# Kernel tuning notes

Measured on AMD Instinct MI355X. Metric: run time of the kernel, lower is better.

## Reference

```python
import jax, jax.numpy as jnp
import numpy as np

HEAD_DIM = 64
N_HEADS = 25
N_KV_HEADS = 5
WINDOW = 1024
N_META = 128
EPS = 1e-6
ROPE_BASE = 10000.0


def _rmsnorm(x, w):
    # per-head RMSNorm over last dim, computed in fp32 (matches HymbaRMSNorm)
    xf = x.astype(jnp.float32)
    var = jnp.mean(xf * xf, axis=-1, keepdims=True)
    return w * (xf * jax.lax.rsqrt(var + EPS)).astype(x.dtype)


def _rotate_half(x):
    x1, x2 = jnp.split(x, 2, axis=-1)
    return jnp.concatenate((-x2, x1), axis=-1)


def _rope_cos_sin(position_ids):
    # equivalent to indexing the cached cos/sin tables with position_ids
    inv_freq = 1.0 / (ROPE_BASE ** (jnp.arange(0, HEAD_DIM, 2, dtype=jnp.float32) / HEAD_DIM))
    freqs = position_ids.astype(jnp.float32)[..., None] * inv_freq  # [B,T,hd/2]
    emb = jnp.concatenate((freqs, freqs), axis=-1)                   # [B,T,hd]
    return jnp.cos(emb)[:, None], jnp.sin(emb)[:, None]              # [B,1,T,hd]


def setup_inputs() -> dict:
    key = jax.random.key(0)
    k1, k2, k3, k4, k5 = jax.random.split(key, 5)
    B, T = 2, 2048
    return {
        "query_states": jax.random.normal(k1, (B, T, N_HEADS * HEAD_DIM), dtype=jnp.float32),
        "key_states": jax.random.normal(k2, (B, T, N_KV_HEADS * HEAD_DIM), dtype=jnp.float32),
        "value_states": jax.random.normal(k3, (B, T, N_KV_HEADS * HEAD_DIM), dtype=jnp.float32),
        "q_norm_w": jax.random.uniform(k4, (HEAD_DIM,), dtype=jnp.float32, minval=0.5, maxval=1.5),
        "k_norm_w": jax.random.uniform(k5, (HEAD_DIM,), dtype=jnp.float32, minval=0.5, maxval=1.5),
        "position_ids": jnp.broadcast_to(jnp.arange(T, dtype=jnp.int32), (B, T)),
    }


def reference(query_states, key_states, value_states, q_norm_w, k_norm_w, position_ids):
    B, T, _ = query_states.shape
    # [B, H, T, hd]
    q = query_states.reshape(B, T, N_HEADS, HEAD_DIM).transpose(0, 2, 1, 3)
    k = key_states.reshape(B, T, N_KV_HEADS, HEAD_DIM).transpose(0, 2, 1, 3)
    v = value_states.reshape(B, T, N_KV_HEADS, HEAD_DIM).transpose(0, 2, 1, 3)

    # per-head QK RMSNorm
    q = _rmsnorm(q, q_norm_w)
    k = _rmsnorm(k, k_norm_w)

    # RoPE
    cos, sin = _rope_cos_sin(position_ids)
    q = q * cos + _rotate_half(q) * sin
    k = k * cos + _rotate_half(k) * sin

    # GQA: repeat each kv head num_heads // num_kv_heads times (consecutively)
    n_rep = N_HEADS // N_KV_HEADS
    k_e = jnp.repeat(k, n_rep, axis=1)
    v_e = jnp.repeat(v, n_rep, axis=1)

    scale = 1.0 / np.sqrt(HEAD_DIM)
    scores = jnp.einsum("bhqd,bhkd->bhqk", q, k_e) * scale

    # SWA mask: causal AND (in sliding window OR meta/memory token)
    q_idx = jnp.arange(T)[:, None]
    k_idx = jnp.arange(T)[None, :]
    attend = (k_idx <= q_idx) & ((k_idx >= q_idx - WINDOW + 1) | (k_idx < N_META))
    scores = jnp.where(attend, scores, -jnp.inf)

    attn_weights = jax.nn.softmax(scores, axis=-1)
    out = jnp.einsum("bhqk,bhkd->bhqd", attn_weights, v_e)
    return out.transpose(0, 2, 1, 3).reshape(B, T, N_HEADS * HEAD_DIM)
```

## Files before the change

### kernel.cpp

```cpp
#include <hip/hip_runtime.h>
#include <cmath>

typedef float  f32x4  __attribute__((ext_vector_type(4)));
typedef __bf16 bf16x8 __attribute__((ext_vector_type(8)));
typedef unsigned int u32x4 __attribute__((ext_vector_type(4)));
typedef unsigned int u32x2 __attribute__((ext_vector_type(2)));
typedef unsigned int   u32;
typedef unsigned short u16;

#define HEAD_DIM 64
#define N_HEADS  25
#define N_KV     5
#define WINDOW   1024
#define N_META   128
#define B_       2
#define T_       2048
#define QB       64
#define NTILES   (T_ / 64)
#define TILE_U32 2048
#define SM_BIAS  (-20.0f)

static __device__ __forceinline__ u16 bf16_bits(float f) {
  __bf16 h = (__bf16)f;
  return __builtin_bit_cast(u16, h);
}
static __device__ __forceinline__ u32 pack2(float lo, float hi) {
  return ((u32)bf16_bits(hi) << 16) | bf16_bits(lo);
}
static __device__ __forceinline__ float fexp2(float x) {
  return __builtin_amdgcn_exp2f(x);
}
static __device__ __forceinline__ void gload16(const u32* g, u32* l) {
  __builtin_amdgcn_global_load_lds((const __attribute__((address_space(1))) u32*)g,
                                   (__attribute__((address_space(3))) u32*)l, 16, 0, 0);
}

__global__ __launch_bounds__(256) void prep_kernel(
    const float* __restrict__ k_in, const float* __restrict__ k_w,
    const float* __restrict__ v_in, const int* __restrict__ pos_ids,
    u32* __restrict__ k_ws, u32* __restrict__ v_ws)
{
  const int blk = blockIdx.x;
  const int tid = threadIdx.x;

  if (blk < B_ * N_KV * NTILES) {
    int tile = blk & (NTILES - 1);
    int bk   = blk >> 5;
    int kvh  = bk % N_KV, b = bk / N_KV;
    int t0   = tile * 64;

    __shared__ u16 Tl[64][72];

    #pragma unroll
    for (int it = 0; it < 4; ++it) {
      int idx = it * 256 + tid;
      int kl = idx >> 4, dq = idx & 15;
      const float4 f = *(const float4*)&v_in[((size_t)(b * T_ + t0 + kl)) * (N_KV * HEAD_DIM) + kvh * HEAD_DIM + dq * 4];
      Tl[dq * 4 + 0][kl] = bf16_bits(f.x);
      Tl[dq * 4 + 1][kl] = bf16_bits(f.y);
      Tl[dq * 4 + 2][kl] = bf16_bits(f.z);
      Tl[dq * 4 + 3][kl] = bf16_bits(f.w);
    }
    __syncthreads();

    u32* outb = v_ws + (size_t)blk * TILE_U32;
    #pragma unroll
    for (int it = 0; it < 8; ++it) {
      int o = it * 256 + tid;
      int d = o >> 5, c = o & 31;
      u32 w = ((u32)Tl[d][2 * c + 1] << 16) | Tl[d][2 * c];
      int a = c >> 4, bs = (c >> 3) & 1, gp = (c >> 1) & 3, e = c & 1;
      int sp = (4 * a + gp) ^ (d & 7);
      outb[d * 32 + sp * 4 + 2 * bs + e] = w;
    }
    return;
  }

  const int lane = tid & 63, wid = tid >> 6;
  const int l15 = lane & 15, g = lane >> 4;
  const int gw   = (blk - B_ * N_KV * NTILES) * 4 + wid;
  const int bkvh = gw >> 7;
  const int sl   = gw & 127;
  const int b    = bkvh / N_KV, kvh = bkvh % N_KV;
  const int t0   = sl * 16;

  const int   jbase = (4 * l15) & 31;
  const float r32   = 0.74989420933f;
  float fr[4];
  fr[0] = powf(10000.f, -(float)jbase * (1.f / 32.f));
  fr[1] = fr[0] * r32; fr[2] = fr[1] * r32; fr[3] = fr[2] * r32;

  const int t0g = b * T_ + t0;
  int pos_prev = pos_ids[t0g + g];
  float cc[4], sn[4], c4[4], s4[4];
  #pragma unroll
  for (int e = 0; e < 4; ++e) {
    sincosf((float)pos_prev * fr[e], &sn[e], &cc[e]);
    sincosf(4.f * fr[e], &s4[e], &c4[e]);
  }
  const float4 wv = *(const float4*)&k_w[4 * l15];
  u32* outb = k_ws + ((size_t)bkvh * NTILES + (t0 >> 6)) * TILE_U32;
  const int klbase = t0 & 63;
  const int sp_c   = l15 >> 1;
  const int slot   = (2 * l15) & 3;

  #pragma unroll
  for (int it = 0; it < 4; ++it) {
    const int row = 4 * it + g;
    if (it) {
      int pos = pos_ids[t0g + row];
      if (__all(pos == pos_prev + 4)) {
        #pragma unroll
        for (int e = 0; e < 4; ++e) {
          float c2 = cc[e] * c4[e] - sn[e] * s4[e];
          sn[e] = sn[e] * c4[e] + cc[e] * s4[e];
          cc[e] = c2;
        }
      } else {
        #pragma unroll
        for (int e = 0; e < 4; ++e) sincosf((float)pos * fr[e], &sn[e], &cc[e]);
      }
      pos_prev = pos;
    }
    const float4 xv = *(const float4*)&k_in[((size_t)(t0g + row)) * (N_KV * HEAD_DIM) + kvh * HEAD_DIM + 4 * l15];
    float ss = xv.x * xv.x + xv.y * xv.y + xv.z * xv.z + xv.w * xv.w;
    ss += __shfl_xor(ss, 1); ss += __shfl_xor(ss, 2);
    ss += __shfl_xor(ss, 4); ss += __shfl_xor(ss, 8);
    const float rn = rsqrtf(ss * (1.f / 64.f) + 1e-6f);
    float y[4] = {wv.x * xv.x * rn, wv.y * xv.y * rn, wv.z * xv.z * rn, wv.w * xv.w * rn};
    float rv[4];
    #pragma unroll
    for (int e = 0; e < 4; ++e) {
      float part = __shfl_xor(y[e], 8);
      rv[e] = (l15 < 8) ? (y[e] * cc[e] - part * sn[e])
                        : (y[e] * cc[e] + part * sn[e]);
    }
    const int kl = klbase + row;
    const int sp = sp_c ^ (kl & 7);
    u32x2 w2;
    w2.x = pack2(rv[0], rv[1]);
    w2.y = pack2(rv[2], rv[3]);
    *(u32x2*)&outb[kl * 32 + sp * 4 + slot] = w2;
  }
}

__global__ __launch_bounds__(256, 4) void attn_kernel(
    const float* __restrict__ q_in, const float* __restrict__ q_w,
    const int* __restrict__ pos_ids,
    const u32* __restrict__ kws, const u32* __restrict__ vws,
    float* __restrict__ out)
{
  const int i  = blockIdx.x;
  const int x  = i & 7;
  int k = i >> 3;
  {
    const int row = k >> 5, col = k & 31;
    const int base = row * 32;
    const int span = (200 - base < 32) ? (200 - base) : 32;
    k = base + ((row & 1) ? (span - 1 - col) : col);
  }
  const int gA = (5 * x) >> 2;
  const int a0 = 200 * x - 160 * gA;
  const int nB = 40 + a0;
  int grp, j_;
  if (k < nB) { grp = gA + 1; j_ = k; }
  else        { grp = gA;     j_ = a0 + (k - nB); }
  const int qt  = 31 - j_ / 5;
  const int hh  = j_ % 5;
  const int b   = grp / 5;
  const int kvh = grp % 5;
  const int h   = kvh * 5 + hh;
  const int qb  = qt * QB;
  const int tid = threadIdx.x, wid = tid >> 6, lane = tid & 63;
  const int l15 = lane & 15, g = lane >> 4;
  const int qrow0 = wid * 16;

  __shared__ u32 Ks[TILE_U32];
  __shared__ u32 Vt[TILE_U32];

  const int nt    = (qt <= 18) ? (qt + 1) : 19;
  const int shift = qt - 18;

  const size_t kvbase = ((size_t)(b * N_KV + kvh)) * NTILES * TILE_U32;
  const u32* kb = kws + kvbase;
  const u32* vb = vws + kvbase;

  #pragma unroll
  for (int j = 0; j < 2; ++j) {
    int ci = (wid << 1) | j;
    gload16(kb + ci * 256 + lane * 4, &Ks[ci * 256]);
  }

  {
    const int   jbase = (4 * l15) & 31;
    const float r32   = 0.74989420933f;
    float fr[4];
    fr[0] = powf(10000.f, -(float)jbase * (1.f / 32.f));
    fr[1] = fr[0] * r32; fr[2] = fr[1] * r32; fr[3] = fr[2] * r32;

    const int t0g = b * T_ + qb + qrow0;
    int pos_prev = pos_ids[t0g + g];
    float cc[4], sn[4], c4[4], s4[4];
    #pragma unroll
    for (int e = 0; e < 4; ++e) {
      sincosf((float)pos_prev * fr[e], &sn[e], &cc[e]);
      sincosf(4.f * fr[e], &s4[e], &c4[e]);
    }
    const float4 wv = *(const float4*)&q_w[4 * l15];
    #pragma unroll
    for (int it = 0; it < 4; ++it) {
      const int row = 4 * it + g;
      if (it) {
        int pos = pos_ids[t0g + row];
        if (__all(pos == pos_prev + 4)) {
          #pragma unroll
          for (int e = 0; e < 4; ++e) {
            float c2 = cc[e] * c4[e] - sn[e] * s4[e];
            sn[e] = sn[e] * c4[e] + cc[e] * s4[e];
            cc[e] = c2;
          }
        } else {
          #pragma unroll
          for (int e = 0; e < 4; ++e) sincosf((float)pos * fr[e], &sn[e], &cc[e]);
        }
        pos_prev = pos;
      }
      const float4 xv = *(const float4*)&q_in[((size_t)(t0g + row)) * (N_HEADS * HEAD_DIM) + h * HEAD_DIM + 4 * l15];
      float ss = xv.x * xv.x + xv.y * xv.y + xv.z * xv.z + xv.w * xv.w;
      ss += __shfl_xor(ss, 1); ss += __shfl_xor(ss, 2);
      ss += __shfl_xor(ss, 4); ss += __shfl_xor(ss, 8);
      const float rn = rsqrtf(ss * (1.f / 64.f) + 1e-6f);
      float y[4] = {wv.x * xv.x * rn, wv.y * xv.y * rn, wv.z * xv.z * rn, wv.w * xv.w * rn};
      float rv[4];
      #pragma unroll
      for (int e = 0; e < 4; ++e) {
        float part = __shfl_xor(y[e], 8);
        rv[e] = ((l15 < 8) ? (y[e] * cc[e] - part * sn[e])
                           : (y[e] * cc[e] + part * sn[e])) * 0.18033688f;
      }
      u32x2 w2;
      w2.x = pack2(rv[0], rv[1]);
      w2.y = pack2(rv[2], rv[3]);
      *(u32x2*)&Vt[(qrow0 + row) * 32 + 2 * l15] = w2;
    }
  }
  __syncthreads();

  bf16x8 qf[2];
  #pragma unroll
  for (int ks = 0; ks < 2; ++ks)
    qf[ks] = *(const bf16x8*)&Vt[(qrow0 + l15) * 32 + 16 * ks + 4 * g];
  __syncthreads();

  #pragma unroll
  for (int j = 0; j < 2; ++j) {
    int ci = (wid << 1) | j;
    gload16(vb + ci * 256 + lane * 4, &Vt[ci * 256]);
  }

  f32x4 acc_o[4];
  #pragma unroll
  for (int mt = 0; mt < 4; ++mt) acc_o[mt] = (f32x4)(0.f);
  f32x4 acc_l = (f32x4)(0.f);

  u32x4 onesw;
  onesw.x = 0x3F803F80u; onesw.y = 0x3F803F80u; onesw.z = 0x3F803F80u; onesw.w = 0x3F803F80u;
  const bf16x8 vones = __builtin_bit_cast(bf16x8, onesw);

  const int q_abs = qb + qrow0 + l15;

  for (int i2 = 0; i2 < nt; ++i2) {
    const int k0 = ((qt <= 18 || i2 < 2) ? i2 : i2 + shift) << 6;
    int tn = -1;
    if (i2 + 1 < nt) tn = (qt <= 18 || i2 + 1 < 2) ? (i2 + 1) : (i2 + 1 + shift);

    f32x4 accs[4];
    #pragma unroll
    for (int mt = 0; mt < 4; ++mt) accs[mt] = (f32x4)(SM_BIAS);
    #pragma unroll
    for (int ks = 0; ks < 2; ++ks) {
      #pragma unroll
      for (int mt = 0; mt < 4; ++mt) {
        bf16x8 kf = *(const bf16x8*)&Ks[(16 * mt + l15) * 32 + (((4 * ks + g) ^ (l15 & 7)) << 2)];
        accs[mt] = __builtin_amdgcn_mfma_f32_16x16x32_bf16(kf, qf[ks], accs[mt], 0, 0, 0);
      }
    }

    const bool do_mask = (i2 == nt - 1) || (qt >= 18 && i2 == 2);
    if (do_mask) {
      #pragma unroll
      for (int mt = 0; mt < 4; ++mt)
        #pragma unroll
        for (int rg = 0; rg < 4; ++rg) {
          int key = k0 + 16 * mt + 4 * g + rg;
          bool ok = (key <= q_abs) && ((key >= q_abs - (WINDOW - 1)) || (key < N_META));
          accs[mt][rg] = ok ? accs[mt][rg] : -INFINITY;
        }
    }
    #pragma unroll
    for (int mt = 0; mt < 4; ++mt)
      #pragma unroll
      for (int rg = 0; rg < 4; ++rg)
        accs[mt][rg] = fexp2(accs[mt][rg]);

    __syncthreads();

    if (tn >= 0) {
      const u32* kt = kb + (size_t)tn * TILE_U32;
      #pragma unroll
      for (int j = 0; j < 2; ++j) {
        int ci = (wid << 1) | j;
        gload16(kt + ci * 256 + lane * 4, &Ks[ci * 256]);
      }
    }

    #pragma unroll
    for (int ks2 = 0; ks2 < 2; ++ks2) {
      const int m0 = 2 * ks2, m1 = 2 * ks2 + 1;
      u32x4 aw;
      aw.x = pack2(accs[m0][0], accs[m0][1]);
      aw.y = pack2(accs[m0][2], accs[m0][3]);
      aw.z = pack2(accs[m1][0], accs[m1][1]);
      aw.w = pack2(accs[m1][2], accs[m1][3]);
      bf16x8 af = __builtin_bit_cast(bf16x8, aw);
      acc_l = __builtin_amdgcn_mfma_f32_16x16x32_bf16(af, vones, acc_l, 0, 0, 0);
      #pragma unroll
      for (int mt2 = 0; mt2 < 4; ++mt2) {
        bf16x8 vf = *(const bf16x8*)&Vt[(16 * mt2 + l15) * 32 + (((4 * ks2 + g) ^ (l15 & 7)) << 2)];
        acc_o[mt2] = __builtin_amdgcn_mfma_f32_16x16x32_bf16(af, vf, acc_o[mt2], 0, 0, 0);
      }
    }

    __syncthreads();

    if (tn >= 0) {
      const u32* vt = vb + (size_t)tn * TILE_U32;
      #pragma unroll
      for (int j = 0; j < 2; ++j) {
        int ci = (wid << 1) | j;
        gload16(vt + ci * 256 + lane * 4, &Vt[ci * 256]);
      }
    }
  }

  #pragma unroll
  for (int mt2 = 0; mt2 < 4; ++mt2)
    #pragma unroll
    for (int rg = 0; rg < 4; ++rg) {
      int t = qb + qrow0 + 4 * g + rg;
      out[((size_t)(b * T_ + t)) * (N_HEADS * HEAD_DIM) + h * HEAD_DIM + 16 * mt2 + l15] =
          acc_o[mt2][rg] / acc_l[rg];
    }
}

extern "C" void kernel_launch(void* const* d_in, const int* in_sizes, int n_in,
                              void* d_out, int out_size, void* d_ws, size_t ws_size,
                              hipStream_t stream) {
  const float* q   = (const float*)d_in[0];
  const float* k   = (const float*)d_in[1];
  const float* v   = (const float*)d_in[2];
  const float* qw  = (const float*)d_in[3];
  const float* kw  = (const float*)d_in[4];
  const int*   pos = (const int*)d_in[5];

  u32* kp = (u32*)d_ws;
  u32* vp = kp + (size_t)B_ * N_KV * NTILES * TILE_U32;
  float* outp = (float*)d_out;

  prep_kernel<<<2 * B_ * N_KV * NTILES, 256, 0, stream>>>(k, kw, v, pos, kp, vp);
  attn_kernel<<<1600, 256, 0, stream>>>(q, qw, pos, kp, vp, outp);
}
```

Baseline: 52.38 us.

## Double-buffer K tiles in LDS and read V fragments directly from global

Replaces the single K and V shared-memory tiles with a double-buffered K tile, so the next K tile is prefetched into the alternate buffer while the current one is used. V fragments are now loaded straight from global memory into registers at the start of each iteration, using precomputed swizzled offsets, instead of being staged through LDS. This drops one of the two barriers per iteration. The cost is more register pressure and uncoalesced 16-byte global loads for V that rely on cache hits. Whether the prefetch of K is safe with a single barrier depends on gload16's async semantics.

```diff
diff --git a/kernel.cpp b/kernel.cpp
--- a/kernel.cpp
+++ b/kernel.cpp
@@ -175,8 +175,7 @@
   const int l15 = lane & 15, g = lane >> 4;
   const int qrow0 = wid * 16;
 
-  __shared__ u32 Ks[TILE_U32];
-  __shared__ u32 Vt[TILE_U32];
+  __shared__ u32 Ks[2 * TILE_U32];
 
   const int nt    = (qt <= 18) ? (qt + 1) : 19;
   const int shift = qt - 18;
@@ -241,7 +240,7 @@
       u32x2 w2;
       w2.x = pack2(rv[0], rv[1]);
       w2.y = pack2(rv[2], rv[3]);
-      *(u32x2*)&Vt[(qrow0 + row) * 32 + 2 * l15] = w2;
+      *(u32x2*)&Ks[TILE_U32 + (qrow0 + row) * 32 + 2 * l15] = w2;
     }
   }
   __syncthreads();
@@ -249,14 +248,15 @@
   bf16x8 qf[2];
   #pragma unroll
   for (int ks = 0; ks < 2; ++ks)
-    qf[ks] = *(const bf16x8*)&Vt[(qrow0 + l15) * 32 + 16 * ks + 4 * g];
+    qf[ks] = *(const bf16x8*)&Ks[TILE_U32 + (qrow0 + l15) * 32 + 16 * ks + 4 * g];
   __syncthreads();
 
-  #pragma unroll
-  for (int j = 0; j < 2; ++j) {
-    int ci = (wid << 1) | j;
-    gload16(vb + ci * 256 + lane * 4, &Vt[ci * 256]);
-  }
+  int voff[2][4];
+  #pragma unroll
+  for (int ks2 = 0; ks2 < 2; ++ks2)
+    #pragma unroll
+    for (int mt2 = 0; mt2 < 4; ++mt2)
+      voff[ks2][mt2] = (16 * mt2 + l15) * 32 + (((4 * ks2 + g) ^ (l15 & 7)) << 2);
 
   f32x4 acc_o[4];
   #pragma unroll
@@ -270,9 +270,28 @@
   const int q_abs = qb + qrow0 + l15;
 
   for (int i2 = 0; i2 < nt; ++i2) {
-    const int k0 = ((qt <= 18 || i2 < 2) ? i2 : i2 + shift) << 6;
-    int tn = -1;
-    if (i2 + 1 < nt) tn = (qt <= 18 || i2 + 1 < 2) ? (i2 + 1) : (i2 + 1 + shift);
+    const int buf  = i2 & 1;
+    const int tval = (qt <= 18 || i2 < 2) ? i2 : i2 + shift;
+    const int k0   = tval << 6;
+
+    const u32* vtile = vb + (size_t)tval * TILE_U32;
+    bf16x8 vf[2][4];
+    #pragma unroll
+    for (int ks2 = 0; ks2 < 2; ++ks2)
+      #pragma unroll
+      for (int mt2 = 0; mt2 < 4; ++mt2)
+        vf[ks2][mt2] = *(const bf16x8*)&vtile[voff[ks2][mt2]];
+
+    if (i2 + 1 < nt) {
+      int tn = (qt <= 18 || i2 + 1 < 2) ? (i2 + 1) : (i2 + 1 + shift);
+      const u32* kt = kb + (size_t)tn * TILE_U32;
+      u32* kd = &Ks[(buf ^ 1) * TILE_U32];
+      #pragma unroll
+      for (int j = 0; j < 2; ++j) {
+        int ci = (wid << 1) | j;
+        gload16(kt + ci * 256 + lane * 4, kd + ci * 256);
+      }
+    }
 
     f32x4 accs[4];
     #pragma unroll
@@ -281,7 +300,7 @@
     for (int ks = 0; ks < 2; ++ks) {
       #pragma unroll
       for (int mt = 0; mt < 4; ++mt) {
-        bf16x8 kf = *(const bf16x8*)&Ks[(16 * mt + l15) * 32 + (((4 * ks + g) ^ (l15 & 7)) << 2)];
+        bf16x8 kf = *(const bf16x8*)&Ks[buf * TILE_U32 + (16 * mt + l15) * 32 + (((4 * ks + g) ^ (l15 & 7)) << 2)];
         accs[mt] = __builtin_amdgcn_mfma_f32_16x16x32_bf16(kf, qf[ks], accs[mt], 0, 0, 0);
       }
     }
@@ -302,17 +321,6 @@
       #pragma unroll
       for (int rg = 0; rg < 4; ++rg)
         accs[mt][rg] = fexp2(accs[mt][rg]);
-
-    __syncthreads();
-
-    if (tn >= 0) {
-      const u32* kt = kb + (size_t)tn * TILE_U32;
-      #pragma unroll
-      for (int j = 0; j < 2; ++j) {
-        int ci = (wid << 1) | j;
-        gload16(kt + ci * 256 + lane * 4, &Ks[ci * 256]);
-      }
-    }
 
     #pragma unroll
     for (int ks2 = 0; ks2 < 2; ++ks2) {
@@ -325,22 +333,11 @@
       bf16x8 af = __builtin_bit_cast(bf16x8, aw);
       acc_l = __builtin_amdgcn_mfma_f32_16x16x32_bf16(af, vones, acc_l, 0, 0, 0);
       #pragma unroll
-      for (int mt2 = 0; mt2 < 4; ++mt2) {
-        bf16x8 vf = *(const bf16x8*)&Vt[(16 * mt2 + l15) * 32 + (((4 * ks2 + g) ^ (l15 & 7)) << 2)];
-        acc_o[mt2] = __builtin_amdgcn_mfma_f32_16x16x32_bf16(af, vf, acc_o[mt2], 0, 0, 0);
-      }
+      for (int mt2 = 0; mt2 < 4; ++mt2)
+        acc_o[mt2] = __builtin_amdgcn_mfma_f32_16x16x32_bf16(af, vf[ks2][mt2], acc_o[mt2], 0, 0, 0);
     }
 
     __syncthreads();
-
-    if (tn >= 0) {
-      const u32* vt = vb + (size_t)tn * TILE_U32;
-      #pragma unroll
-      for (int j = 0; j < 2; ++j) {
-        int ci = (wid << 1) | j;
-        gload16(vt + ci * 256 + lane * 4, &Vt[ci * 256]);
-      }
-    }
   }
 
   #pragma unroll
```

New measurement: 63.90 us. 22.0% more time.
